# Kernel optimization log

Hardware: AMD Instinct MI355X
Metric: run time of the kernel (lower is better)

## Reference

```python
import math
import jax, jax.numpy as jnp
import numpy as np

G = 128        # graphs per batch
N0 = 512       # nodes per graph
H = 256        # hidden size
E = 524288     # edges (avg degree 8), intra-graph
RATIO = 0.8


def setup_inputs() -> dict:
    key = jax.random.key(0)
    ks = jax.random.split(key, 16)
    # intra-graph edges: E//G edges per graph
    eg = jnp.arange(E, dtype=jnp.int32) // (E // G)
    src = eg * N0 + jax.random.randint(ks[0], (E,), 0, N0, dtype=jnp.int32)
    dst = eg * N0 + jax.random.randint(ks[1], (E,), 0, N0, dtype=jnp.int32)
    s = 1.0 / math.sqrt(H)
    return {
        "x": jax.random.normal(ks[2], (G * N0, H), jnp.float32),
        "edge_src": src,
        "edge_dst": dst,
        "W_in": jax.random.normal(ks[3], (H, H), jnp.float32) * s,
        "b_in": jnp.zeros((H,), jnp.float32),
        "W_h0": jax.random.normal(ks[4], (H, H), jnp.float32) * s,
        "b_h0": jnp.zeros((H,), jnp.float32),
        "W_h1": jax.random.normal(ks[5], (H, H), jnp.float32) * s,
        "b_h1": jnp.zeros((H,), jnp.float32),
        "p_in": jax.random.normal(ks[6], (H,), jnp.float32),
        "p_h0": jax.random.normal(ks[7], (H,), jnp.float32),
        "p_h1": jax.random.normal(ks[8], (H,), jnp.float32),
        "att_w": jax.random.normal(ks[9], (H,), jnp.float32) * s,
        "att_b": jnp.zeros((1,), jnp.float32),
    }


def gcn_conv(x, W, b, src, dst, emask, num_nodes):
    # PyG GCNConv: lin -> sym-normalized propagate (with self loops, weight 1) -> bias
    h = x @ W
    deg = jax.ops.segment_sum(emask, dst, num_segments=num_nodes) + 1.0  # +1 self loop
    dis = jax.lax.rsqrt(deg)
    coef = dis[src] * dis[dst] * emask                    # [E]
    agg = jax.ops.segment_sum(h[src] * coef[:, None], dst, num_segments=num_nodes)
    agg = agg + h * (dis * dis)[:, None]                  # self-loop message
    return agg + b


def topk_pool(x, p, src, dst, emask, n_cur):
    # PyG TopKPooling: score = tanh(x.p/|p|), keep top ceil(ratio*n) per graph,
    # x' = x[perm]*score[perm], edges filtered to kept nodes and remapped.
    k = int(math.ceil(RATIO * n_cur))
    score = jnp.tanh((x @ p) / jnp.linalg.norm(p))        # [G*n_cur]
    _, idx = jax.lax.top_k(score.reshape(G, n_cur), k)    # [G,k]
    perm = (idx + (jnp.arange(G, dtype=idx.dtype) * n_cur)[:, None]).reshape(-1)
    x_new = x[perm] * score[perm][:, None]                # [G*k,H]
    mapping = jnp.full((G * n_cur,), -1, jnp.int32).at[perm].set(
        jnp.arange(G * k, dtype=jnp.int32))
    ns, nd = mapping[src], mapping[dst]
    valid = (ns >= 0) & (nd >= 0) & (emask > 0)
    return (x_new, jnp.where(valid, ns, 0), jnp.where(valid, nd, 0),
            valid.astype(x.dtype), k)


def att_pool(x, att_w, att_b, k):
    # GlobalAttention: per-graph softmax gate, weighted sum
    gate = (x @ att_w + att_b[0]).reshape(G, k)
    att = jax.nn.softmax(gate, axis=1)
    return jnp.einsum('gk,gkh->gh', att, x.reshape(G, k, H))


def reference(x, edge_src, edge_dst, W_in, b_in, W_h0, b_h0, W_h1, b_h1,
              p_in, p_h0, p_h1, att_w, att_b):
    src, dst = edge_src, edge_dst
    emask = jnp.ones((E,), x.dtype)
    n_cur = N0
    h = jax.nn.relu(gcn_conv(x, W_in, b_in, src, dst, emask, G * n_cur))
    h, src, dst, emask, n_cur = topk_pool(h, p_in, src, dst, emask, n_cur)
    out = att_pool(h, att_w, att_b, n_cur)
    for (W, b, p) in ((W_h0, b_h0, p_h0), (W_h1, b_h1, p_h1)):
        h = jax.nn.relu(gcn_conv(h, W, b, src, dst, emask, G * n_cur))
        h, src, dst, emask, n_cur = topk_pool(h, p, src, dst, emask, n_cur)
        out = out + att_pool(h, att_w, att_b, n_cur)
    return out  # [G, H]
```

## Files before the change

### kernel.cpp

```cpp
#include <hip/hip_runtime.h>
#include <cmath>

#define G_ 128
#define N0_ 512
#define H_ 256
#define E_ 524288
#define NODES0 (G_*N0_)

typedef _Float16 v8h __attribute__((ext_vector_type(8)));
typedef _Float16 v4h __attribute__((ext_vector_type(4)));
typedef float v4f __attribute__((ext_vector_type(4)));

#define TSTRIDE 72
#define TILEHW (128*TSTRIDE)

__device__ __forceinline__ void async_copy16(void* lds, const void* g) {
  __builtin_amdgcn_global_load_lds(
      (const __attribute__((address_space(1))) void*)g,
      (__attribute__((address_space(3))) void*)lds, 16, 0, 0);
}

__device__ __forceinline__ float4 f4fma(float4 a, float s, float4 acc) {
  acc.x = fmaf(a.x, s, acc.x); acc.y = fmaf(a.y, s, acc.y);
  acc.z = fmaf(a.z, s, acc.z); acc.w = fmaf(a.w, s, acc.w);
  return acc;
}

__device__ __forceinline__ float block_reduce_sum(float v, volatile float* red) {
  #pragma unroll
  for (int off = 32; off > 0; off >>= 1) v += __shfl_down(v, off);
  int lane = threadIdx.x & 63, wid = threadIdx.x >> 6;
  __syncthreads();
  if (lane == 0) red[wid] = v;
  __syncthreads();
  return red[0] + red[1] + red[2] + red[3];
}

__global__ __launch_bounds__(256) void pnorm_kernel(const float* __restrict__ p0,
                                                    const float* __restrict__ p1,
                                                    const float* __restrict__ p2,
                                                    float* __restrict__ pinv) {
  __shared__ float red[4];
  const float* p = (blockIdx.x == 0) ? p0 : (blockIdx.x == 1 ? p1 : p2);
  float v = p[threadIdx.x];
  float s = block_reduce_sum(v * v, red);
  if (threadIdx.x == 0) pinv[blockIdx.x] = 1.0f / sqrtf(s);
}

__global__ void init_cum_kernel(int* __restrict__ cum, int* __restrict__ cnt, int n) {
  int v = blockIdx.x * 256 + threadIdx.x;
  if (v < n) { cum[v] = v; cnt[v] = 0; }
}

__global__ __launch_bounds__(256) void wconv_kernel(const float* __restrict__ W0,
                                                    const float* __restrict__ W1,
                                                    const float* __restrict__ W2,
                                                    _Float16* __restrict__ img) {
  int l = blockIdx.x >> 4;
  const float* W = (l == 0) ? W0 : (l == 1 ? W1 : W2);
  int bn = (blockIdx.x >> 3) & 1, kt = blockIdx.x & 7;
  int t = threadIdx.x;
  int n = t & 127, kh = t >> 7;
  int k0 = kt * 32 + kh * 16;
  _Float16* row = img + (size_t)l * 16 * TILEHW + ((size_t)(bn * 8 + kt) * 128 + n) * TSTRIDE;
  #pragma unroll
  for (int s = 0; s < 2; ++s) {
    v8h hv, lv;
    #pragma unroll
    for (int j = 0; j < 8; ++j) {
      float a = W[(size_t)(k0 + s * 8 + j) * 256 + bn * 128 + n];
      _Float16 h = (_Float16)a;
      hv[j] = h;
      lv[j] = (_Float16)(a - (float)h);
    }
    *(v8h*)&row[kh * 16 + s * 8] = hv;
    *(v8h*)&row[32 + kh * 16 + s * 8] = lv;
  }
}

__global__ __launch_bounds__(256) void gemm_f16x3_kernel(const float* __restrict__ A,
                                                         const _Float16* __restrict__ Wimg,
                                                         float* __restrict__ C) {
  __shared__ _Float16 As[2][TILEHW];
  __shared__ _Float16 Ws[2][TILEHW];
  const int tid = threadIdx.x;
  const int bm = blockIdx.x >> 1;
  const int bn = blockIdx.x & 1;
  const int lane = tid & 63, wid = tid >> 6;
  const int wm = wid >> 1, wn = wid & 1;
  const int l15 = lane & 15, kg = lane >> 4;

  v4f acc[4][4];
  #pragma unroll
  for (int i = 0; i < 4; ++i)
    #pragma unroll
    for (int j = 0; j < 4; ++j) acc[i][j] = (v4f){0.f, 0.f, 0.f, 0.f};

  int arow[4], acc4[4];
  const float* aptr[4];
  #pragma unroll
  for (int i = 0; i < 4; ++i) {
    int c = tid + 256 * i;
    arow[i] = c >> 3;
    acc4[i] = c & 7;
    aptr[i] = A + (size_t)(bm * 128 + arow[i]) * 256 + acc4[i] * 4;
  }
  const _Float16* wtile0 = Wimg + (size_t)bn * 8 * TILEHW;

  float4 pa[4];

  auto issueW = [&](int kt, int buf) {
    const _Float16* wt = wtile0 + (size_t)kt * TILEHW;
    #pragma unroll
    for (int cb = 0; cb < 5; ++cb) {
      int c = wid + cb * 4;
      if (c < 18) async_copy16(&Ws[buf][c * 512], wt + (size_t)c * 512 + lane * 8);
    }
  };
  auto convertA = [&](int buf) {
    #pragma unroll
    for (int i = 0; i < 4; ++i) {
      float av[4] = {pa[i].x, pa[i].y, pa[i].z, pa[i].w};
      v4h hv, lv;
      #pragma unroll
      for (int j = 0; j < 4; ++j) {
        _Float16 h = (_Float16)av[j];
        hv[j] = h;
        lv[j] = (_Float16)(av[j] - (float)h);
      }
      _Float16* dst = &As[buf][arow[i] * TSTRIDE + acc4[i] * 4];
      *(v4h*)(dst) = hv;
      *(v4h*)(dst + 32) = lv;
    }
  };
  auto loadA = [&](int kt) {
    #pragma unroll
    for (int i = 0; i < 4; ++i) pa[i] = *(const float4*)(aptr[i] + kt * 32);
  };

  loadA(0);
  issueW(0, 0);
  convertA(0);
  loadA(1);
  __syncthreads();

  for (int kt = 0; kt < 8; ++kt) {
    int cur = kt & 1;
    if (kt < 7) {
      issueW(kt + 1, cur ^ 1);
      convertA(cur ^ 1);
      if (kt < 6) loadA(kt + 2);
    }
    v8h ah[4], bh[4], al[4], bl[4];
    #pragma unroll
    for (int i = 0; i < 4; ++i)
      ah[i] = *(const v8h*)&As[cur][(wm * 64 + i * 16 + l15) * TSTRIDE + kg * 8];
    #pragma unroll
    for (int j = 0; j < 4; ++j)
      bh[j] = *(const v8h*)&Ws[cur][(wn * 64 + j * 16 + l15) * TSTRIDE + kg * 8];
    #pragma unroll
    for (int i = 0; i < 4; ++i)
      #pragma unroll
      for (int j = 0; j < 4; ++j)
        acc[i][j] = __builtin_amdgcn_mfma_f32_16x16x32_f16(ah[i], bh[j], acc[i][j], 0, 0, 0);
    #pragma unroll
    for (int i = 0; i < 4; ++i)
      al[i] = *(const v8h*)&As[cur][(wm * 64 + i * 16 + l15) * TSTRIDE + 32 + kg * 8];
    #pragma unroll
    for (int i = 0; i < 4; ++i)
      #pragma unroll
      for (int j = 0; j < 4; ++j)
        acc[i][j] = __builtin_amdgcn_mfma_f32_16x16x32_f16(al[i], bh[j], acc[i][j], 0, 0, 0);
    #pragma unroll
    for (int j = 0; j < 4; ++j)
      bl[j] = *(const v8h*)&Ws[cur][(wn * 64 + j * 16 + l15) * TSTRIDE + 32 + kg * 8];
    #pragma unroll
    for (int i = 0; i < 4; ++i)
      #pragma unroll
      for (int j = 0; j < 4; ++j)
        acc[i][j] = __builtin_amdgcn_mfma_f32_16x16x32_f16(ah[i], bl[j], acc[i][j], 0, 0, 0);
    if (kt < 7) __syncthreads();
  }

  #pragma unroll
  for (int i = 0; i < 4; ++i) {
    #pragma unroll
    for (int j = 0; j < 4; ++j) {
      #pragma unroll
      for (int r = 0; r < 4; ++r) {
        int row = bm * 128 + wm * 64 + i * 16 + kg * 4 + r;
        int col = bn * 128 + wn * 64 + j * 16 + l15;
        C[(size_t)row * 256 + col] = acc[i][j][r];
      }
    }
  }
}

__global__ void count_deg_kernel(const int* __restrict__ esrc, const int* __restrict__ edst,
                                 const int* __restrict__ cum, int* __restrict__ cnt) {
  int e = blockIdx.x * 256 + threadIdx.x;
  if (e >= E_) return;
  int ms = cum[esrc[e]], md = cum[edst[e]];
  if (ms >= 0 && md >= 0) atomicAdd(&cnt[md], 1);
}

__global__ __launch_bounds__(256) void scan1_kernel(const int* __restrict__ cnt,
                                                    int* __restrict__ row_start,
                                                    int* __restrict__ bsum,
                                                    float* __restrict__ dis,
                                                    int* __restrict__ cursor, int n) {
  __shared__ int sdata[256];
  int base = blockIdx.x * 1024;
  int t = threadIdx.x;
  int v[4]; int s = 0;
  #pragma unroll
  for (int i = 0; i < 4; ++i) {
    int idx = base + t * 4 + i;
    v[i] = (idx < n) ? cnt[idx] : 0;
    s += v[i];
    if (idx < n) {
      dis[idx] = 1.0f / sqrtf((float)v[i] + 1.0f);
      cursor[idx] = 0;
    }
  }
  sdata[t] = s;
  __syncthreads();
  for (int off = 1; off < 256; off <<= 1) {
    int x = (t >= off) ? sdata[t - off] : 0;
    __syncthreads();
    sdata[t] += x;
    __syncthreads();
  }
  int excl = sdata[t] - s;
  if (t == 255) bsum[blockIdx.x] = sdata[255];
  #pragma unroll
  for (int i = 0; i < 4; ++i) {
    int idx = base + t * 4 + i;
    if (idx < n) { row_start[idx] = excl; excl += v[i]; }
  }
}

__global__ __launch_bounds__(256) void scan2_kernel(int* __restrict__ bsum,
                                                    int* __restrict__ row_start, int nb, int n) {
  __shared__ int sdata[256];
  int t = threadIdx.x;
  int v = (t < nb) ? bsum[t] : 0;
  sdata[t] = v;
  __syncthreads();
  for (int off = 1; off < 256; off <<= 1) {
    int x = (t >= off) ? sdata[t - off] : 0;
    __syncthreads();
    sdata[t] += x;
    __syncthreads();
  }
  if (t < nb) bsum[t] = sdata[t] - v;
  if (t == 255) row_start[n] = sdata[255];
}

__global__ void scan3_kernel(int* __restrict__ row_start, const int* __restrict__ bsum,
                             int* __restrict__ cnt, int n) {
  int idx = blockIdx.x * 256 + threadIdx.x;
  if (idx < n) { row_start[idx] += bsum[idx >> 10]; cnt[idx] = 0; }
}

__global__ void fill_csr_kernel(const int* __restrict__ esrc, const int* __restrict__ edst,
                                const int* __restrict__ cum, const int* __restrict__ row_start,
                                int* __restrict__ cursor, const float* __restrict__ dis,
                                int* __restrict__ csr_src, float* __restrict__ csr_cf) {
  int e = blockIdx.x * 256 + threadIdx.x;
  if (e >= E_) return;
  int ms = cum[esrc[e]], md = cum[edst[e]];
  if (ms < 0 || md < 0) return;
  int pos = atomicAdd(&cursor[md], 1);
  int j = row_start[md] + pos;
  csr_src[j] = ms;
  csr_cf[j] = dis[ms] * dis[md];
}

__global__ __launch_bounds__(256) void agg_score_kernel(
    const float4* __restrict__ hlin4, const float* __restrict__ dis,
    const float4* __restrict__ bias4,
    const int* __restrict__ row_start, const int* __restrict__ csr_src,
    const float* __restrict__ csr_cf, const float4* __restrict__ p4,
    const float* __restrict__ pinvp,
    float4* __restrict__ hout4, float* __restrict__ score, int q) {
  int blk = (blockIdx.x & 7) * q + (blockIdx.x >> 3);
  int wave = threadIdx.x >> 6, lane = threadIdx.x & 63;
  int v = blk * 4 + wave;
  float dv = dis[v];
  float self = dv * dv;
  float4 h = hlin4[(size_t)v * 64 + lane];
  float4 acc = make_float4(h.x * self, h.y * self, h.z * self, h.w * self);
  int rs = row_start[v], re = row_start[v + 1];
  int j = rs;
  for (; j + 8 <= re; j += 8) {
    int s[8]; float c[8]; float4 hh[8];
    #pragma unroll
    for (int u = 0; u < 8; ++u) { s[u] = csr_src[j + u]; c[u] = csr_cf[j + u]; }
    #pragma unroll
    for (int u = 0; u < 8; ++u) hh[u] = hlin4[(size_t)s[u] * 64 + lane];
    #pragma unroll
    for (int u = 0; u < 8; ++u) acc = f4fma(hh[u], c[u], acc);
  }
  if (j + 4 <= re) {
    int s[4]; float c[4]; float4 hh[4];
    #pragma unroll
    for (int u = 0; u < 4; ++u) { s[u] = csr_src[j + u]; c[u] = csr_cf[j + u]; }
    #pragma unroll
    for (int u = 0; u < 4; ++u) hh[u] = hlin4[(size_t)s[u] * 64 + lane];
    #pragma unroll
    for (int u = 0; u < 4; ++u) acc = f4fma(hh[u], c[u], acc);
    j += 4;
  }
  for (; j < re; ++j) {
    acc = f4fma(hlin4[(size_t)csr_src[j] * 64 + lane], csr_cf[j], acc);
  }
  float4 b = bias4[lane];
  acc.x = fmaxf(acc.x + b.x, 0.0f); acc.y = fmaxf(acc.y + b.y, 0.0f);
  acc.z = fmaxf(acc.z + b.z, 0.0f); acc.w = fmaxf(acc.w + b.w, 0.0f);
  hout4[(size_t)v * 64 + lane] = acc;
  float4 pv = p4[lane];
  float s = acc.x * pv.x + acc.y * pv.y + acc.z * pv.z + acc.w * pv.w;
  #pragma unroll
  for (int off = 32; off > 0; off >>= 1) s += __shfl_down(s, off);
  if (lane == 0) score[v] = tanhf(s * pinvp[0]);
}

__global__ __launch_bounds__(256) void topk_kernel(const float* __restrict__ score, int n, int k,
                                                   int* __restrict__ cum, int* __restrict__ perm) {
  __shared__ float key[512];
  __shared__ int kid[512];
  __shared__ int newmap[512];
  int g = blockIdx.x, t = threadIdx.x;
  for (int i = t; i < 512; i += 256) {
    key[i] = (i < n) ? score[(size_t)g * n + i] : -INFINITY;
    kid[i] = i;
    if (i < n) newmap[i] = -1;
  }
  __syncthreads();
  for (int kk = 2; kk <= 512; kk <<= 1) {
    for (int j = kk >> 1; j > 0; j >>= 1) {
      #pragma unroll
      for (int half = 0; half < 2; ++half) {
        int i = t + half * 256;
        int ixj = i ^ j;
        if (ixj > i) {
          float ka = key[i]; int ia = kid[i];
          float kb = key[ixj]; int ib = kid[ixj];
          bool b_first = (kb > ka) || (kb == ka && ib < ia);
          bool sw = ((i & kk) == 0) ? b_first : !b_first;
          if (sw) { key[i] = kb; kid[i] = ib; key[ixj] = ka; kid[ixj] = ia; }
        }
      }
      __syncthreads();
    }
  }
  for (int i = t; i < k; i += 256) {
    int local = kid[i];
    perm[g * k + i] = g * n + local;
    newmap[local] = g * k + i;
  }
  __syncthreads();
  #pragma unroll
  for (int u = 0; u < N0_ / 256; ++u) {
    int v = g * N0_ + u * 256 + t;
    int c = cum[v];
    if (c >= 0) cum[v] = newmap[c - g * n];
  }
}

__global__ __launch_bounds__(256) void gather_gate_kernel(
    const float4* __restrict__ h4, const float* __restrict__ score, const int* __restrict__ perm,
    const float4* __restrict__ attw4, const float* __restrict__ attb,
    float4* __restrict__ xnew4, float* __restrict__ gate, int q) {
  int blk = (blockIdx.x & 7) * q + (blockIdx.x >> 3);
  int wave = threadIdx.x >> 6, lane = threadIdx.x & 63;
  int i = blk * 4 + wave;
  int s = perm[i];
  float sc = score[s];
  float4 h = h4[(size_t)s * 64 + lane];
  float4 val = make_float4(h.x * sc, h.y * sc, h.z * sc, h.w * sc);
  xnew4[(size_t)i * 64 + lane] = val;
  float4 aw = attw4[lane];
  float g = val.x * aw.x + val.y * aw.y + val.z * aw.z + val.w * aw.w;
  #pragma unroll
  for (int off = 32; off > 0; off >>= 1) g += __shfl_down(g, off);
  if (lane == 0) gate[i] = g + attb[0];
}

__global__ __launch_bounds__(512) void att_pool_kernel(const float4* __restrict__ x4,
                                                       const float* __restrict__ gate,
                                                       float* __restrict__ out, int k, int add) {
  __shared__ float att[512];
  __shared__ float red[8];
  __shared__ float4 part[512];
  int g = blockIdx.x, t = threadIdx.x;
  int wave = t >> 6, lane = t & 63;
  const float* gg = gate + (size_t)g * k;

  float m = -INFINITY;
  for (int i = t; i < k; i += 512) m = fmaxf(m, gg[i]);
  #pragma unroll
  for (int off = 32; off > 0; off >>= 1) m = fmaxf(m, __shfl_down(m, off));
  if (lane == 0) red[wave] = m;
  __syncthreads();
  m = red[0];
  #pragma unroll
  for (int w = 1; w < 8; ++w) m = fmaxf(m, red[w]);
  __syncthreads();

  float s = 0.0f;
  for (int i = t; i < k; i += 512) {
    float e = expf(gg[i] - m);
    att[i] = e;
    s += e;
  }
  #pragma unroll
  for (int off = 32; off > 0; off >>= 1) s += __shfl_down(s, off);
  if (lane == 0) red[wave] = s;
  __syncthreads();
  s = red[0] + red[1] + red[2] + red[3] + red[4] + red[5] + red[6] + red[7];
  float inv = 1.0f / s;

  float4 acc = make_float4(0.f, 0.f, 0.f, 0.f);
  const float4* xg = x4 + (size_t)g * k * 64;
  for (int i = wave; i < k; i += 8) acc = f4fma(xg[(size_t)i * 64 + lane], att[i], acc);
  part[t] = acc;
  __syncthreads();
  if (wave == 0) {
    float4 r = part[lane];
    #pragma unroll
    for (int w = 1; w < 8; ++w) {
      float4 pw = part[w * 64 + lane];
      r.x += pw.x; r.y += pw.y; r.z += pw.z; r.w += pw.w;
    }
    r.x *= inv; r.y *= inv; r.z *= inv; r.w *= inv;
    float4* o4 = (float4*)out + (size_t)g * 64 + lane;
    if (add) {
      float4 prev = *o4;
      r.x += prev.x; r.y += prev.y; r.z += prev.z; r.w += prev.w;
    }
    *o4 = r;
  }
}

extern "C" void kernel_launch(void* const* d_in, const int* in_sizes, int n_in,
                              void* d_out, int out_size, void* d_ws, size_t ws_size,
                              hipStream_t stream) {
  const float* x    = (const float*)d_in[0];
  const int*   esrc = (const int*)d_in[1];
  const int*   edst = (const int*)d_in[2];
  const float* Wl[3] = {(const float*)d_in[3], (const float*)d_in[5], (const float*)d_in[7]};
  const float* bl[3] = {(const float*)d_in[4], (const float*)d_in[6], (const float*)d_in[8]};
  const float* pl[3] = {(const float*)d_in[9], (const float*)d_in[10], (const float*)d_in[11]};
  const float* attw = (const float*)d_in[12];
  const float* attb = (const float*)d_in[13];
  float* out = (float*)d_out;

  char* w = (char*)d_ws;
  auto carve = [&](size_t bytes) { char* p = w; w += (bytes + 255) & ~(size_t)255; return p; };
  float* bufA    = (float*)carve((size_t)NODES0 * H_ * 4);
  float* bufB    = (float*)carve((size_t)NODES0 * H_ * 4);
  int*   csr_src = (int*)  carve((size_t)E_ * 4);
  float* csr_cf  = (float*)carve((size_t)E_ * 4);
  int*   cnt     = (int*)  carve((size_t)NODES0 * 4);
  int*   row_st  = (int*)  carve((size_t)(NODES0 + 1) * 4);
  int*   cursor  = (int*)  carve((size_t)NODES0 * 4);
  float* dis     = (float*)carve((size_t)NODES0 * 4);
  float* score   = (float*)carve((size_t)NODES0 * 4);
  int*   cum_map = (int*)  carve((size_t)NODES0 * 4);
  int*   perm    = (int*)  carve((size_t)NODES0 * 4);
  float* gate    = (float*)carve((size_t)NODES0 * 4);
  int*   bsum    = (int*)  carve(256 * 4);
  float* pinv    = (float*)carve(16);
  _Float16* Wimg = (_Float16*)carve((size_t)3 * 16 * TILEHW * 2);
  (void)ws_size; (void)in_sizes; (void)n_in; (void)out_size;

  pnorm_kernel<<<3, 256, 0, stream>>>(pl[0], pl[1], pl[2], pinv);
  init_cum_kernel<<<NODES0 / 256, 256, 0, stream>>>(cum_map, cnt, NODES0);
  wconv_kernel<<<48, 256, 0, stream>>>(Wl[0], Wl[1], Wl[2], Wimg);

  int n_cur = N0_;
  const float* xin = x;
  for (int l = 0; l < 3; ++l) {
    int nodes = G_ * n_cur;
    float* hlin = (l & 1) ? bufB : bufA;
    float* hbuf = (l & 1) ? bufA : bufB;
    float* xnew = hlin;

    gemm_f16x3_kernel<<<(nodes / 128) * 2, 256, 0, stream>>>(
        xin, Wimg + (size_t)l * 16 * TILEHW, hlin);

    count_deg_kernel<<<E_ / 256, 256, 0, stream>>>(esrc, edst, cum_map, cnt);
    int nb = (nodes + 1023) / 1024;
    scan1_kernel<<<nb, 256, 0, stream>>>(cnt, row_st, bsum, dis, cursor, nodes);
    scan2_kernel<<<1, 256, 0, stream>>>(bsum, row_st, nb, nodes);
    scan3_kernel<<<(nodes + 255) / 256, 256, 0, stream>>>(row_st, bsum, cnt, nodes);
    fill_csr_kernel<<<E_ / 256, 256, 0, stream>>>(esrc, edst, cum_map, row_st, cursor, dis,
                                                  csr_src, csr_cf);

    int agg_blocks = nodes / 4;
    agg_score_kernel<<<agg_blocks, 256, 0, stream>>>(
        (const float4*)hlin, dis, (const float4*)bl[l], row_st, csr_src, csr_cf,
        (const float4*)pl[l], pinv + l, (float4*)hbuf, score, agg_blocks / 8);

    int kk = (int)std::ceil(0.8 * (double)n_cur);
    topk_kernel<<<G_, 256, 0, stream>>>(score, n_cur, kk, cum_map, perm);
    int rows = G_ * kk;
    int gg_blocks = rows / 4;
    gather_gate_kernel<<<gg_blocks, 256, 0, stream>>>(
        (const float4*)hbuf, score, perm, (const float4*)attw, attb,
        (float4*)xnew, gate, gg_blocks / 8);

    att_pool_kernel<<<G_, 512, 0, stream>>>((const float4*)xnew, gate, out, kk, l > 0 ? 1 : 0);

    n_cur = kk;
    xin = xnew;
  }
}
```

Baseline: 449.6 us.

## Fuse gather/gate/attention pooling, fold scan3 into consumers, single-buffer GEMM LDS

Merges the gather-gate and attention-pool kernels into one per-graph kernel that uses an online softmax, so gate values no longer make a round trip through global memory. It also removes the scan3 pass by adding block offsets inside fill_csr and agg_score, with agg_score clearing cnt. The GEMM moves from double-buffered to single-buffered LDS, which costs overlap but halves LDS use and may allow more blocks per CU. The fused pool runs only 128 blocks, so parallelism for the gather falls sharply.

```diff
diff --git a/kernel.cpp b/kernel.cpp
--- a/kernel.cpp
+++ b/kernel.cpp
@@ -81,8 +81,8 @@
 __global__ __launch_bounds__(256) void gemm_f16x3_kernel(const float* __restrict__ A,
                                                          const _Float16* __restrict__ Wimg,
                                                          float* __restrict__ C) {
-  __shared__ _Float16 As[2][TILEHW];
-  __shared__ _Float16 Ws[2][TILEHW];
+  __shared__ _Float16 As[TILEHW];
+  __shared__ _Float16 Ws[TILEHW];
   const int tid = threadIdx.x;
   const int bm = blockIdx.x >> 1;
   const int bn = blockIdx.x & 1;
@@ -108,16 +108,15 @@
   const _Float16* wtile0 = Wimg + (size_t)bn * 8 * TILEHW;
 
   float4 pa[4];
-
-  auto issueW = [&](int kt, int buf) {
-    const _Float16* wt = wtile0 + (size_t)kt * TILEHW;
-    #pragma unroll
-    for (int cb = 0; cb < 5; ++cb) {
-      int c = wid + cb * 4;
-      if (c < 18) async_copy16(&Ws[buf][c * 512], wt + (size_t)c * 512 + lane * 8);
-    }
-  };
-  auto convertA = [&](int buf) {
+  #pragma unroll
+  for (int i = 0; i < 4; ++i) pa[i] = *(const float4*)(aptr[i] + 0);
+
+  for (int kt = 0; kt < 8; ++kt) {
+    {
+      const _Float16* wt = wtile0 + (size_t)kt * TILEHW;
+      for (int cb = wid; cb < 18; cb += 4)
+        async_copy16(&Ws[cb * 512], wt + (size_t)cb * 512 + lane * 8);
+    }
     #pragma unroll
     for (int i = 0; i < 4; ++i) {
       float av[4] = {pa[i].x, pa[i].y, pa[i].z, pa[i].w};
@@ -128,36 +127,25 @@
         hv[j] = h;
         lv[j] = (_Float16)(av[j] - (float)h);
       }
-      _Float16* dst = &As[buf][arow[i] * TSTRIDE + acc4[i] * 4];
+      _Float16* dst = &As[arow[i] * TSTRIDE + acc4[i] * 4];
       *(v4h*)(dst) = hv;
       *(v4h*)(dst + 32) = lv;
     }
-  };
-  auto loadA = [&](int kt) {
-    #pragma unroll
-    for (int i = 0; i < 4; ++i) pa[i] = *(const float4*)(aptr[i] + kt * 32);
-  };
-
-  loadA(0);
-  issueW(0, 0);
-  convertA(0);
-  loadA(1);
-  __syncthreads();
-
-  for (int kt = 0; kt < 8; ++kt) {
-    int cur = kt & 1;
+    __syncthreads();
+
     if (kt < 7) {
-      issueW(kt + 1, cur ^ 1);
-      convertA(cur ^ 1);
-      if (kt < 6) loadA(kt + 2);
-    }
+      #pragma unroll
+      for (int i = 0; i < 4; ++i)
+        pa[i] = *(const float4*)(aptr[i] + (kt + 1) * 32);
+    }
+
     v8h ah[4], bh[4], al[4], bl[4];
     #pragma unroll
     for (int i = 0; i < 4; ++i)
-      ah[i] = *(const v8h*)&As[cur][(wm * 64 + i * 16 + l15) * TSTRIDE + kg * 8];
+      ah[i] = *(const v8h*)&As[(wm * 64 + i * 16 + l15) * TSTRIDE + kg * 8];
     #pragma unroll
     for (int j = 0; j < 4; ++j)
-      bh[j] = *(const v8h*)&Ws[cur][(wn * 64 + j * 16 + l15) * TSTRIDE + kg * 8];
+      bh[j] = *(const v8h*)&Ws[(wn * 64 + j * 16 + l15) * TSTRIDE + kg * 8];
     #pragma unroll
     for (int i = 0; i < 4; ++i)
       #pragma unroll
@@ -165,7 +153,7 @@
         acc[i][j] = __builtin_amdgcn_mfma_f32_16x16x32_f16(ah[i], bh[j], acc[i][j], 0, 0, 0);
     #pragma unroll
     for (int i = 0; i < 4; ++i)
-      al[i] = *(const v8h*)&As[cur][(wm * 64 + i * 16 + l15) * TSTRIDE + 32 + kg * 8];
+      al[i] = *(const v8h*)&As[(wm * 64 + i * 16 + l15) * TSTRIDE + 32 + kg * 8];
     #pragma unroll
     for (int i = 0; i < 4; ++i)
       #pragma unroll
@@ -173,13 +161,13 @@
         acc[i][j] = __builtin_amdgcn_mfma_f32_16x16x32_f16(al[i], bh[j], acc[i][j], 0, 0, 0);
     #pragma unroll
     for (int j = 0; j < 4; ++j)
-      bl[j] = *(const v8h*)&Ws[cur][(wn * 64 + j * 16 + l15) * TSTRIDE + 32 + kg * 8];
+      bl[j] = *(const v8h*)&Ws[(wn * 64 + j * 16 + l15) * TSTRIDE + 32 + kg * 8];
     #pragma unroll
     for (int i = 0; i < 4; ++i)
       #pragma unroll
       for (int j = 0; j < 4; ++j)
         acc[i][j] = __builtin_amdgcn_mfma_f32_16x16x32_f16(ah[i], bl[j], acc[i][j], 0, 0, 0);
-    if (kt < 7) __syncthreads();
+    __syncthreads();
   }
 
   #pragma unroll
@@ -257,14 +245,9 @@
   if (t == 255) row_start[n] = sdata[255];
 }
 
-__global__ void scan3_kernel(int* __restrict__ row_start, const int* __restrict__ bsum,
-                             int* __restrict__ cnt, int n) {
-  int idx = blockIdx.x * 256 + threadIdx.x;
-  if (idx < n) { row_start[idx] += bsum[idx >> 10]; cnt[idx] = 0; }
-}
-
 __global__ void fill_csr_kernel(const int* __restrict__ esrc, const int* __restrict__ edst,
                                 const int* __restrict__ cum, const int* __restrict__ row_start,
+                                const int* __restrict__ bsum,
                                 int* __restrict__ cursor, const float* __restrict__ dis,
                                 int* __restrict__ csr_src, float* __restrict__ csr_cf) {
   int e = blockIdx.x * 256 + threadIdx.x;
@@ -272,7 +255,7 @@
   int ms = cum[esrc[e]], md = cum[edst[e]];
   if (ms < 0 || md < 0) return;
   int pos = atomicAdd(&cursor[md], 1);
-  int j = row_start[md] + pos;
+  int j = row_start[md] + bsum[md >> 10] + pos;
   csr_src[j] = ms;
   csr_cf[j] = dis[ms] * dis[md];
 }
@@ -280,10 +263,12 @@
 __global__ __launch_bounds__(256) void agg_score_kernel(
     const float4* __restrict__ hlin4, const float* __restrict__ dis,
     const float4* __restrict__ bias4,
-    const int* __restrict__ row_start, const int* __restrict__ csr_src,
+    const int* __restrict__ row_start, const int* __restrict__ bsum,
+    const int* __restrict__ csr_src,
     const float* __restrict__ csr_cf, const float4* __restrict__ p4,
     const float* __restrict__ pinvp,
-    float4* __restrict__ hout4, float* __restrict__ score, int q) {
+    float4* __restrict__ hout4, float* __restrict__ score,
+    int* __restrict__ cnt, int n, int q) {
   int blk = (blockIdx.x & 7) * q + (blockIdx.x >> 3);
   int wave = threadIdx.x >> 6, lane = threadIdx.x & 63;
   int v = blk * 4 + wave;
@@ -291,7 +276,10 @@
   float self = dv * dv;
   float4 h = hlin4[(size_t)v * 64 + lane];
   float4 acc = make_float4(h.x * self, h.y * self, h.z * self, h.w * self);
-  int rs = row_start[v], re = row_start[v + 1];
+  int rs = row_start[v] + bsum[v >> 10];
+  int v1 = v + 1;
+  int re = row_start[v1] + ((v1 < n) ? bsum[v1 >> 10] : 0);
+  if (lane == 0) cnt[v] = 0;
   int j = rs;
   for (; j + 8 <= re; j += 8) {
     int s[8]; float c[8]; float4 hh[8];
@@ -369,78 +357,62 @@
   }
 }
 
-__global__ __launch_bounds__(256) void gather_gate_kernel(
-    const float4* __restrict__ h4, const float* __restrict__ score, const int* __restrict__ perm,
+__global__ __launch_bounds__(512) void pool_kernel(
+    const float4* __restrict__ h4, const float* __restrict__ score,
+    const int* __restrict__ perm,
     const float4* __restrict__ attw4, const float* __restrict__ attb,
-    float4* __restrict__ xnew4, float* __restrict__ gate, int q) {
-  int blk = (blockIdx.x & 7) * q + (blockIdx.x >> 3);
-  int wave = threadIdx.x >> 6, lane = threadIdx.x & 63;
-  int i = blk * 4 + wave;
-  int s = perm[i];
-  float sc = score[s];
-  float4 h = h4[(size_t)s * 64 + lane];
-  float4 val = make_float4(h.x * sc, h.y * sc, h.z * sc, h.w * sc);
-  xnew4[(size_t)i * 64 + lane] = val;
-  float4 aw = attw4[lane];
-  float g = val.x * aw.x + val.y * aw.y + val.z * aw.z + val.w * aw.w;
-  #pragma unroll
-  for (int off = 32; off > 0; off >>= 1) g += __shfl_down(g, off);
-  if (lane == 0) gate[i] = g + attb[0];
-}
-
-__global__ __launch_bounds__(512) void att_pool_kernel(const float4* __restrict__ x4,
-                                                       const float* __restrict__ gate,
-                                                       float* __restrict__ out, int k, int add) {
-  __shared__ float att[512];
-  __shared__ float red[8];
-  __shared__ float4 part[512];
+    float4* __restrict__ xnew4, float* __restrict__ out, int k, int add) {
+  __shared__ float wmax[8], wsum[8];
+  __shared__ float4 waccs[8][64];
   int g = blockIdx.x, t = threadIdx.x;
   int wave = t >> 6, lane = t & 63;
-  const float* gg = gate + (size_t)g * k;
-
-  float m = -INFINITY;
-  for (int i = t; i < k; i += 512) m = fmaxf(m, gg[i]);
-  #pragma unroll
-  for (int off = 32; off > 0; off >>= 1) m = fmaxf(m, __shfl_down(m, off));
-  if (lane == 0) red[wave] = m;
-  __syncthreads();
-  m = red[0];
-  #pragma unroll
-  for (int w = 1; w < 8; ++w) m = fmaxf(m, red[w]);
-  __syncthreads();
-
-  float s = 0.0f;
-  for (int i = t; i < k; i += 512) {
-    float e = expf(gg[i] - m);
-    att[i] = e;
-    s += e;
-  }
-  #pragma unroll
-  for (int off = 32; off > 0; off >>= 1) s += __shfl_down(s, off);
-  if (lane == 0) red[wave] = s;
-  __syncthreads();
-  s = red[0] + red[1] + red[2] + red[3] + red[4] + red[5] + red[6] + red[7];
-  float inv = 1.0f / s;
-
+  float4 aw = attw4[lane];
+  float ab = attb[0];
+
+  float m = -INFINITY, ssum = 0.0f;
   float4 acc = make_float4(0.f, 0.f, 0.f, 0.f);
-  const float4* xg = x4 + (size_t)g * k * 64;
-  for (int i = wave; i < k; i += 8) acc = f4fma(xg[(size_t)i * 64 + lane], att[i], acc);
-  part[t] = acc;
+  for (int i = wave; i < k; i += 8) {
+    int s = perm[g * k + i];
+    float sc = score[s];
+    float4 hv = h4[(size_t)s * 64 + lane];
+    float4 val = make_float4(hv.x * sc, hv.y * sc, hv.z * sc, hv.w * sc);
+    xnew4[((size_t)g * k + i) * 64 + lane] = val;
+    float gd = val.x * aw.x + val.y * aw.y + val.z * aw.z + val.w * aw.w;
+    #pragma unroll
+    for (int off = 32; off > 0; off >>= 1) gd += __shfl_xor(gd, off);
+    float gi = gd + ab;
+    float mnew = fmaxf(m, gi);
+    float f = __expf(m - mnew);
+    float e = __expf(gi - mnew);
+    acc.x = acc.x * f + val.x * e; acc.y = acc.y * f + val.y * e;
+    acc.z = acc.z * f + val.z * e; acc.w = acc.w * f + val.w * e;
+    ssum = ssum * f + e;
+    m = mnew;
+  }
+  if (lane == 0) { wmax[wave] = m; wsum[wave] = ssum; }
+  waccs[wave][lane] = acc;
   __syncthreads();
   if (wave == 0) {
-    float4 r = part[lane];
-    #pragma unroll
-    for (int w = 1; w < 8; ++w) {
-      float4 pw = part[w * 64 + lane];
-      r.x += pw.x; r.y += pw.y; r.z += pw.z; r.w += pw.w;
-    }
-    r.x *= inv; r.y *= inv; r.z *= inv; r.w *= inv;
+    float mstar = wmax[0];
+    #pragma unroll
+    for (int w = 1; w < 8; ++w) mstar = fmaxf(mstar, wmax[w]);
+    float stot = 0.0f;
+    float4 a = make_float4(0.f, 0.f, 0.f, 0.f);
+    #pragma unroll
+    for (int w = 0; w < 8; ++w) {
+      float sc = __expf(wmax[w] - mstar);
+      stot += wsum[w] * sc;
+      float4 wa = waccs[w][lane];
+      a.x += wa.x * sc; a.y += wa.y * sc; a.z += wa.z * sc; a.w += wa.w * sc;
+    }
+    float inv = 1.0f / stot;
+    a.x *= inv; a.y *= inv; a.z *= inv; a.w *= inv;
     float4* o4 = (float4*)out + (size_t)g * 64 + lane;
     if (add) {
       float4 prev = *o4;
-      r.x += prev.x; r.y += prev.y; r.z += prev.z; r.w += prev.w;
-    }
-    *o4 = r;
+      a.x += prev.x; a.y += prev.y; a.z += prev.z; a.w += prev.w;
+    }
+    *o4 = a;
   }
 }
 
@@ -470,7 +442,6 @@
   float* score   = (float*)carve((size_t)NODES0 * 4);
   int*   cum_map = (int*)  carve((size_t)NODES0 * 4);
   int*   perm    = (int*)  carve((size_t)NODES0 * 4);
-  float* gate    = (float*)carve((size_t)NODES0 * 4);
   int*   bsum    = (int*)  carve(256 * 4);
   float* pinv    = (float*)carve(16);
   _Float16* Wimg = (_Float16*)carve((size_t)3 * 16 * TILEHW * 2);
@@ -495,24 +466,20 @@
     int nb = (nodes + 1023) / 1024;
     scan1_kernel<<<nb, 256, 0, stream>>>(cnt, row_st, bsum, dis, cursor, nodes);
     scan2_kernel<<<1, 256, 0, stream>>>(bsum, row_st, nb, nodes);
-    scan3_kernel<<<(nodes + 255) / 256, 256, 0, stream>>>(row_st, bsum, cnt, nodes);
-    fill_csr_kernel<<<E_ / 256, 256, 0, stream>>>(esrc, edst, cum_map, row_st, cursor, dis,
-                                                  csr_src, csr_cf);
+    fill_csr_kernel<<<E_ / 256, 256, 0, stream>>>(esrc, edst, cum_map, row_st, bsum, cursor,
+                                                  dis, csr_src, csr_cf);
 
     int agg_blocks = nodes / 4;
     agg_score_kernel<<<agg_blocks, 256, 0, stream>>>(
-        (const float4*)hlin, dis, (const float4*)bl[l], row_st, csr_src, csr_cf,
-        (const float4*)pl[l], pinv + l, (float4*)hbuf, score, agg_blocks / 8);
+        (const float4*)hlin, dis, (const float4*)bl[l], row_st, bsum, csr_src, csr_cf,
+        (const float4*)pl[l], pinv + l, (float4*)hbuf, score, cnt, nodes, agg_blocks / 8);
 
     int kk = (int)std::ceil(0.8 * (double)n_cur);
     topk_kernel<<<G_, 256, 0, stream>>>(score, n_cur, kk, cum_map, perm);
-    int rows = G_ * kk;
-    int gg_blocks = rows / 4;
-    gather_gate_kernel<<<gg_blocks, 256, 0, stream>>>(
+
+    pool_kernel<<<G_, 512, 0, stream>>>(
         (const float4*)hbuf, score, perm, (const float4*)attw, attb,
-        (float4*)xnew, gate, gg_blocks / 8);
-
-    att_pool_kernel<<<G_, 512, 0, stream>>>((const float4*)xnew, gate, out, kk, l > 0 ? 1 : 0);
+        (float4*)xnew, out, kk, l > 0 ? 1 : 0);
 
     n_cur = kk;
     xin = xnew;
```

New measurement: 443.3 us. Within noise of the previous version (-1.4%).
